# Kernel optimization log

Measured on AMD Instinct MI355X. Metric: run time of the kernel, lower is better.

## Reference

```python
import jax, jax.numpy as jnp
import numpy as np

N_NODES = 20000
N_REL = 16
N_EDGES = 640000
N_HID = 64
N_CLASS = 16
R = 2 * N_REL + 1  # relations after adding inverses + self-loop relation


def setup_inputs() -> dict:
    key = jax.random.key(0)
    k1, k2, k3, k4, k5, k6, k7 = jax.random.split(key, 7)
    src = jax.random.randint(k1, (N_EDGES,), 0, N_NODES)
    rel = jax.random.randint(k2, (N_EDGES,), 0, N_REL)
    dst = jax.random.randint(k3, (N_EDGES,), 0, N_NODES)
    w1 = jax.random.normal(k4, (R, N_NODES, N_HID), dtype=jnp.float32) * 0.02
    b1 = jax.random.normal(k5, (N_HID,), dtype=jnp.float32) * 0.02
    w2 = jax.random.normal(k6, (R, N_HID, N_CLASS), dtype=jnp.float32) * 0.02
    b2 = jax.random.normal(k7, (N_CLASS,), dtype=jnp.float32) * 0.02
    return {"src": src, "rel": rel, "dst": dst, "w1": w1, "b1": b1,
            "w2": w2, "b2": b2, "nnodes": N_NODES, "nrel": N_REL}


def _triples_plus(src, rel, dst, nnodes, nrel):
    # add_inverse_and_self: [original | inverse (r+nrel) | self-loops (r=2*nrel)]
    loop = jnp.arange(nnodes, dtype=src.dtype)
    s = jnp.concatenate([src, dst, loop])
    r = jnp.concatenate([rel, rel + nrel, jnp.full((nnodes,), 2 * nrel, dtype=rel.dtype)])
    o = jnp.concatenate([dst, src, loop])
    return s, r, o


def reference(src, rel, dst, w1, b1, w2, b2, nnodes, nrel):
    E = src.shape[0]
    Rr = 2 * nrel + 1
    RN = Rr * nnodes
    s, r, o = _triples_plus(src, rel, dst, nnodes, nrel)
    ones = jnp.ones(s.shape[0], dtype=jnp.float32)

    # ---- Layer 1: horizontal stacking, featureless ----
    # adj: rows = s, cols = r*N + o; column-wise normalisation with the
    # torch-rgcn sum-swap between original and inverse edge blocks.
    ro = r * nnodes + o
    cnt_ro = jax.ops.segment_sum(ones, ro, num_segments=RN)
    sums = cnt_ro[ro]
    sums = jnp.concatenate([sums[E:2 * E], sums[:E], sums[2 * E:]])
    vals1 = 1.0 / sums
    # output[s] += vals * w1[r, o, :]
    msg1 = vals1[:, None] * w1.reshape(RN, -1)[ro]  # [E_all, nhid]
    h = jax.ops.segment_sum(msg1, s, num_segments=nnodes) + b1
    h = jax.nn.relu(h)

    # ---- Layer 2: vertical stacking ----
    # adj: rows = r*N + s, cols = o; row-wise normalisation.
    rs = r * nnodes + s
    cnt_rs = jax.ops.segment_sum(ones, rs, num_segments=RN)
    vals2 = 1.0 / cnt_rs[rs]
    af = jax.ops.segment_sum(vals2[:, None] * h[o], rs, num_segments=RN)
    af = af.reshape(Rr, nnodes, -1)  # [R, N, nhid]
    out = jnp.einsum('rio,rni->no', w2, af) + b2  # [N, nclass]
    return out
```

## Files before the change

kernel.cpp:

```cpp
#include <hip/hip_runtime.h>

#define NN    20000
#define NRELH 16
#define RTOT  33
#define NHID  64
#define NCLS  16
#define W2PAD 18

typedef unsigned int u32;

__global__ __launch_bounds__(256) void count_kernel(
    const int* __restrict__ src, const int* __restrict__ rel,
    const int* __restrict__ dst, int E,
    int* __restrict__ cntA, int* __restrict__ cntB) {
    int e = blockIdx.x * 256 + threadIdx.x;
    if (e >= E) return;
    int r = rel[e];
    atomicAdd(&cntA[r * NN + dst[e]], 1);
    atomicAdd(&cntB[r * NN + src[e]], 1);
}

__global__ __launch_bounds__(256) void deg_kernel(
    const int* __restrict__ cntA, const int* __restrict__ cntB,
    int* __restrict__ offsets) {
    int n = blockIdx.x * 256 + threadIdx.x;
    if (n >= NN) return;
    int d = 0;
    for (int r = 0; r < NRELH; ++r) d += cntA[r * NN + n] + cntB[r * NN + n];
    offsets[n + 1] = (d + 3) & ~3;
}

__global__ __launch_bounds__(256) void scan_kernel(int* __restrict__ offsets) {
    __shared__ int part[256];
    int t = threadIdx.x;
    const int CH = (NN + 255) / 256;
    int base = t * CH, end = min(base + CH, NN);
    int s = 0;
    for (int n = base; n < end; ++n) s += offsets[n + 1];
    part[t] = s;
    __syncthreads();
    if (t == 0) {
        int run = 0;
        for (int i = 0; i < 256; ++i) { int v = part[i]; part[i] = run; run += v; }
        offsets[0] = 0;
    }
    __syncthreads();
    int run = part[t];
    for (int n = base; n < end; ++n) { run += offsets[n + 1]; offsets[n + 1] = run; }
}

__global__ __launch_bounds__(256) void cursor_pad_kernel(
    const int* __restrict__ cntA, const int* __restrict__ cntB,
    const int* __restrict__ offsets,
    int* __restrict__ curA, int* __restrict__ curB,
    u32* __restrict__ eidx, float* __restrict__ vals) {
    int n = blockIdx.x * 256 + threadIdx.x;
    if (n >= NN) return;
    int p = offsets[n];
    for (int r = 0; r < NRELH; ++r) { curB[r * NN + n] = p; p += cntB[r * NN + n]; }
    for (int r = 0; r < NRELH; ++r) { curA[r * NN + n] = p; p += cntA[r * NN + n]; }
    int pend = offsets[n + 1];
    for (; p < pend; ++p) { eidx[p] = (32u << 15); vals[p] = 0.0f; }
}

__global__ __launch_bounds__(256) void scatter_kernel(
    const int* __restrict__ src, const int* __restrict__ rel,
    const int* __restrict__ dst, int E,
    const int* __restrict__ cntA, const int* __restrict__ cntB,
    int* __restrict__ curA, int* __restrict__ curB,
    u32* __restrict__ eidx, float* __restrict__ vals) {
    int e = blockIdx.x * 256 + threadIdx.x;
    if (e >= E) return;
    int r = rel[e], s0 = src[e], d = dst[e];
    float vb = 1.0f / (float)cntB[r * NN + s0];
    int p1 = atomicAdd(&curB[r * NN + s0], 1);
    eidx[p1] = (u32)d | ((u32)r << 15);
    vals[p1] = vb;
    float va = 1.0f / (float)cntA[r * NN + d];
    int p2 = atomicAdd(&curA[r * NN + d], 1);
    eidx[p2] = (u32)s0 | ((u32)(r + 16) << 15);
    vals[p2] = va;
}

__global__ __launch_bounds__(256) void layer1_gather(
    const u32* __restrict__ eidx, const int* __restrict__ offsets,
    const float* __restrict__ vals,
    const float* __restrict__ w1, const float* __restrict__ b1,
    float* __restrict__ h) {
    int wid  = (blockIdx.x * 256 + threadIdx.x) >> 6;
    int lane = threadIdx.x & 63;
    if (wid >= NN) return;
    int s = wid;
    float acc = w1[(2 * NRELH * NN + s) * NHID + lane];
    int k0 = offsets[s], k1 = offsets[s + 1];
    for (int k = k0; k < k1; k += 4) {
        uint4  e4 = *(const uint4*)&eidx[k];
        float4 v4 = *(const float4*)&vals[k];
        int row0 = (int)(e4.x >> 15) * NN + (int)(e4.x & 0x7FFF);
        int row1 = (int)(e4.y >> 15) * NN + (int)(e4.y & 0x7FFF);
        int row2 = (int)(e4.z >> 15) * NN + (int)(e4.z & 0x7FFF);
        int row3 = (int)(e4.w >> 15) * NN + (int)(e4.w & 0x7FFF);
        float g0 = w1[row0 * NHID + lane];
        float g1 = w1[row1 * NHID + lane];
        float g2 = w1[row2 * NHID + lane];
        float g3 = w1[row3 * NHID + lane];
        acc += v4.x * g0 + v4.y * g1 + v4.z * g2 + v4.w * g3;
    }
    float v = acc + b1[lane];
    h[s * NHID + lane] = v > 0.0f ? v : 0.0f;
}

__global__ __launch_bounds__(1024) void layer2_fold(
    const u32* __restrict__ eidx, const int* __restrict__ offsets,
    const float* __restrict__ vals,
    const float* __restrict__ h, const float* __restrict__ w2,
    const float* __restrict__ b2, float* __restrict__ out) {
    __shared__ float w2L[RTOT * NHID * W2PAD];
    int tid = threadIdx.x;
    for (int idx = tid; idx < RTOT * NHID * NCLS; idx += 1024) {
        int c = idx & 15;
        int ri = idx >> 4;
        w2L[ri * W2PAD + c] = w2[idx];
    }
    __syncthreads();
    int w = tid >> 6, lane = tid & 63;
    for (int s = blockIdx.x * 16 + w; s < NN; s += gridDim.x * 16) {
        float acc16[16];
#pragma unroll
        for (int c = 0; c < 16; ++c) acc16[c] = 0.0f;
        auto FOLD = [&](int r, float a) {
            int b = (r * NHID + lane) * W2PAD;
#pragma unroll
            for (int q = 0; q < 8; ++q) {
                float2 wv = *(const float2*)&w2L[b + 2 * q];
                acc16[2 * q]     += a * wv.x;
                acc16[2 * q + 1] += a * wv.y;
            }
        };
        float hs = h[s * NHID + lane];
        FOLD(32, hs);
        int rcur = 32; float acc = 0.0f;
        int k0 = offsets[s], k1 = offsets[s + 1];
        for (int k = k0; k < k1; k += 4) {
            uint4  e4 = *(const uint4*)&eidx[k];
            float4 v4 = *(const float4*)&vals[k];
            int o0 = e4.x & 0x7FFF, r0 = e4.x >> 15;
            int o1 = e4.y & 0x7FFF, r1 = e4.y >> 15;
            int o2 = e4.z & 0x7FFF, r2 = e4.z >> 15;
            int o3 = e4.w & 0x7FFF, r3 = e4.w >> 15;
            float h0 = h[o0 * NHID + lane];
            float h1 = h[o1 * NHID + lane];
            float h2 = h[o2 * NHID + lane];
            float h3 = h[o3 * NHID + lane];
            if (r0 != rcur) { FOLD(rcur, acc); acc = 0.0f; rcur = r0; } acc += v4.x * h0;
            if (r1 != rcur) { FOLD(rcur, acc); acc = 0.0f; rcur = r1; } acc += v4.y * h1;
            if (r2 != rcur) { FOLD(rcur, acc); acc = 0.0f; rcur = r2; } acc += v4.z * h2;
            if (r3 != rcur) { FOLD(rcur, acc); acc = 0.0f; rcur = r3; } acc += v4.w * h3;
        }
        FOLD(rcur, acc);
        float s8[8];
#pragma unroll
        for (int j = 0; j < 8; ++j) {
            float p0 = __shfl_xor(acc16[2 * j], 1, 64);
            float p1 = __shfl_xor(acc16[2 * j + 1], 1, 64);
            float e0 = acc16[2 * j] + p0, e1 = acc16[2 * j + 1] + p1;
            s8[j] = (lane & 1) ? e1 : e0;
        }
        float s4[4];
#pragma unroll
        for (int j = 0; j < 4; ++j) {
            float p0 = __shfl_xor(s8[2 * j], 2, 64);
            float p1 = __shfl_xor(s8[2 * j + 1], 2, 64);
            float e0 = s8[2 * j] + p0, e1 = s8[2 * j + 1] + p1;
            s4[j] = (lane & 2) ? e1 : e0;
        }
        float s2[2];
#pragma unroll
        for (int j = 0; j < 2; ++j) {
            float p0 = __shfl_xor(s4[2 * j], 4, 64);
            float p1 = __shfl_xor(s4[2 * j + 1], 4, 64);
            float e0 = s4[2 * j] + p0, e1 = s4[2 * j + 1] + p1;
            s2[j] = (lane & 4) ? e1 : e0;
        }
        float p0 = __shfl_xor(s2[0], 8, 64);
        float p1 = __shfl_xor(s2[1], 8, 64);
        float e0 = s2[0] + p0, e1 = s2[1] + p1;
        float t = (lane & 8) ? e1 : e0;
        t += __shfl_xor(t, 16, 64);
        t += __shfl_xor(t, 32, 64);
        if (lane < 16) out[s * NCLS + lane] = t + b2[lane];
    }
}

extern "C" void kernel_launch(void* const* d_in, const int* in_sizes, int n_in,
                              void* d_out, int out_size, void* d_ws, size_t ws_size,
                              hipStream_t stream) {
    const int*   src = (const int*)d_in[0];
    const int*   rel = (const int*)d_in[1];
    const int*   dst = (const int*)d_in[2];
    const float* w1  = (const float*)d_in[3];
    const float* b1  = (const float*)d_in[4];
    const float* w2  = (const float*)d_in[5];
    const float* b2  = (const float*)d_in[6];
    float* out = (float*)d_out;
    const int E = in_sizes[0];
    const int ECAP = 2 * E + 4 * NN;

    int*   cntA    = (int*)d_ws;
    int*   cntB    = cntA + NRELH * NN;
    int*   curA    = cntB + NRELH * NN;
    int*   curB    = curA + NRELH * NN;
    int*   offsets = curB + NRELH * NN;
    u32*   eidx    = (u32*)(offsets + NN + 4);
    float* vals    = (float*)(eidx + ECAP);
    float* h       = vals + ECAP;

    hipMemsetAsync(cntA, 0, (size_t)(2 * NRELH * NN) * 4, stream);

    count_kernel<<<(E + 255) / 256, 256, 0, stream>>>(src, rel, dst, E, cntA, cntB);
    deg_kernel<<<(NN + 255) / 256, 256, 0, stream>>>(cntA, cntB, offsets);
    scan_kernel<<<1, 256, 0, stream>>>(offsets);
    cursor_pad_kernel<<<(NN + 255) / 256, 256, 0, stream>>>(cntA, cntB, offsets,
                                                            curA, curB, eidx, vals);
    scatter_kernel<<<(E + 255) / 256, 256, 0, stream>>>(src, rel, dst, E, cntA, cntB,
                                                        curA, curB, eidx, vals);
    layer1_gather<<<(NN * 64) / 256, 256, 0, stream>>>(eidx, offsets, vals, w1, b1, h);
    layer2_fold<<<256, 1024, 0, stream>>>(eidx, offsets, vals, h, w2, b2, out);
}
```

Measured before the change: 520.9 us.

## Replace CSR scan with atomic bump allocation and interleave edge index/value pairs

The three kernels for degree, single-block scan and cursor setup become one alloc kernel. It reserves each node's padded segment with an atomicAdd on a global counter and stores explicit start and end arrays. This removes the serial one-block scan and two launches. Edge indices and normalisation values are now interleaved as uint2, so the gather kernels fetch both with the same vector loads and the scatter does one 8-byte store per edge. Segment bounds are made wave-uniform with readfirstlane. Node segments are no longer stored in node order, which can reduce locality between neighbouring nodes' edge lists.

Result: faster. 460.5 us (-11.6%).

```diff
diff --git a/kernel.cpp b/kernel.cpp
--- a/kernel.cpp
+++ b/kernel.cpp
@@ -20,47 +20,30 @@
     atomicAdd(&cntB[r * NN + src[e]], 1);
 }
 
-__global__ __launch_bounds__(256) void deg_kernel(
+__global__ __launch_bounds__(256) void alloc_kernel(
     const int* __restrict__ cntA, const int* __restrict__ cntB,
-    int* __restrict__ offsets) {
+    int* __restrict__ gcount,
+    int* __restrict__ curA, int* __restrict__ curB,
+    int* __restrict__ nodeStart, int* __restrict__ nodeEnd,
+    uint2* __restrict__ ent) {
     int n = blockIdx.x * 256 + threadIdx.x;
     if (n >= NN) return;
+    int cb[NRELH], ca[NRELH];
     int d = 0;
-    for (int r = 0; r < NRELH; ++r) d += cntA[r * NN + n] + cntB[r * NN + n];
-    offsets[n + 1] = (d + 3) & ~3;
-}
-
-__global__ __launch_bounds__(256) void scan_kernel(int* __restrict__ offsets) {
-    __shared__ int part[256];
-    int t = threadIdx.x;
-    const int CH = (NN + 255) / 256;
-    int base = t * CH, end = min(base + CH, NN);
-    int s = 0;
-    for (int n = base; n < end; ++n) s += offsets[n + 1];
-    part[t] = s;
-    __syncthreads();
-    if (t == 0) {
-        int run = 0;
-        for (int i = 0; i < 256; ++i) { int v = part[i]; part[i] = run; run += v; }
-        offsets[0] = 0;
-    }
-    __syncthreads();
-    int run = part[t];
-    for (int n = base; n < end; ++n) { run += offsets[n + 1]; offsets[n + 1] = run; }
-}
-
-__global__ __launch_bounds__(256) void cursor_pad_kernel(
-    const int* __restrict__ cntA, const int* __restrict__ cntB,
-    const int* __restrict__ offsets,
-    int* __restrict__ curA, int* __restrict__ curB,
-    u32* __restrict__ eidx, float* __restrict__ vals) {
-    int n = blockIdx.x * 256 + threadIdx.x;
-    if (n >= NN) return;
-    int p = offsets[n];
-    for (int r = 0; r < NRELH; ++r) { curB[r * NN + n] = p; p += cntB[r * NN + n]; }
-    for (int r = 0; r < NRELH; ++r) { curA[r * NN + n] = p; p += cntA[r * NN + n]; }
-    int pend = offsets[n + 1];
-    for (; p < pend; ++p) { eidx[p] = (32u << 15); vals[p] = 0.0f; }
+#pragma unroll
+    for (int r = 0; r < NRELH; ++r) { cb[r] = cntB[r * NN + n]; d += cb[r]; }
+#pragma unroll
+    for (int r = 0; r < NRELH; ++r) { ca[r] = cntA[r * NN + n]; d += ca[r]; }
+    int pdeg = (d + 3) & ~3;
+    int base = atomicAdd(gcount, pdeg);
+    nodeStart[n] = base;
+    nodeEnd[n]   = base + pdeg;
+    int p = base;
+#pragma unroll
+    for (int r = 0; r < NRELH; ++r) { curB[r * NN + n] = p; p += cb[r]; }
+#pragma unroll
+    for (int r = 0; r < NRELH; ++r) { curA[r * NN + n] = p; p += ca[r]; }
+    for (; p < base + pdeg; ++p) ent[p] = make_uint2(32u << 15, 0u);
 }
 
 __global__ __launch_bounds__(256) void scatter_kernel(
@@ -68,51 +51,51 @@
     const int* __restrict__ dst, int E,
     const int* __restrict__ cntA, const int* __restrict__ cntB,
     int* __restrict__ curA, int* __restrict__ curB,
-    u32* __restrict__ eidx, float* __restrict__ vals) {
+    uint2* __restrict__ ent) {
     int e = blockIdx.x * 256 + threadIdx.x;
     if (e >= E) return;
     int r = rel[e], s0 = src[e], d = dst[e];
     float vb = 1.0f / (float)cntB[r * NN + s0];
     int p1 = atomicAdd(&curB[r * NN + s0], 1);
-    eidx[p1] = (u32)d | ((u32)r << 15);
-    vals[p1] = vb;
+    ent[p1] = make_uint2((u32)d | ((u32)r << 15), __float_as_uint(vb));
     float va = 1.0f / (float)cntA[r * NN + d];
     int p2 = atomicAdd(&curA[r * NN + d], 1);
-    eidx[p2] = (u32)s0 | ((u32)(r + 16) << 15);
-    vals[p2] = va;
+    ent[p2] = make_uint2((u32)s0 | ((u32)(r + 16) << 15), __float_as_uint(va));
 }
 
 __global__ __launch_bounds__(256) void layer1_gather(
-    const u32* __restrict__ eidx, const int* __restrict__ offsets,
-    const float* __restrict__ vals,
+    const uint2* __restrict__ ent,
+    const int* __restrict__ nodeStart, const int* __restrict__ nodeEnd,
     const float* __restrict__ w1, const float* __restrict__ b1,
     float* __restrict__ h) {
     int wid  = (blockIdx.x * 256 + threadIdx.x) >> 6;
     int lane = threadIdx.x & 63;
     if (wid >= NN) return;
     int s = wid;
+    int k0 = __builtin_amdgcn_readfirstlane(nodeStart[s]);
+    int k1 = __builtin_amdgcn_readfirstlane(nodeEnd[s]);
     float acc = w1[(2 * NRELH * NN + s) * NHID + lane];
-    int k0 = offsets[s], k1 = offsets[s + 1];
     for (int k = k0; k < k1; k += 4) {
-        uint4  e4 = *(const uint4*)&eidx[k];
-        float4 v4 = *(const float4*)&vals[k];
-        int row0 = (int)(e4.x >> 15) * NN + (int)(e4.x & 0x7FFF);
-        int row1 = (int)(e4.y >> 15) * NN + (int)(e4.y & 0x7FFF);
-        int row2 = (int)(e4.z >> 15) * NN + (int)(e4.z & 0x7FFF);
-        int row3 = (int)(e4.w >> 15) * NN + (int)(e4.w & 0x7FFF);
+        uint4 ea = *(const uint4*)&ent[k];
+        uint4 eb = *(const uint4*)&ent[k + 2];
+        int row0 = (int)(ea.x >> 15) * NN + (int)(ea.x & 0x7FFF);
+        int row1 = (int)(ea.z >> 15) * NN + (int)(ea.z & 0x7FFF);
+        int row2 = (int)(eb.x >> 15) * NN + (int)(eb.x & 0x7FFF);
+        int row3 = (int)(eb.z >> 15) * NN + (int)(eb.z & 0x7FFF);
         float g0 = w1[row0 * NHID + lane];
         float g1 = w1[row1 * NHID + lane];
         float g2 = w1[row2 * NHID + lane];
         float g3 = w1[row3 * NHID + lane];
-        acc += v4.x * g0 + v4.y * g1 + v4.z * g2 + v4.w * g3;
+        acc += __uint_as_float(ea.y) * g0 + __uint_as_float(ea.w) * g1
+             + __uint_as_float(eb.y) * g2 + __uint_as_float(eb.w) * g3;
     }
     float v = acc + b1[lane];
     h[s * NHID + lane] = v > 0.0f ? v : 0.0f;
 }
 
 __global__ __launch_bounds__(1024) void layer2_fold(
-    const u32* __restrict__ eidx, const int* __restrict__ offsets,
-    const float* __restrict__ vals,
+    const uint2* __restrict__ ent,
+    const int* __restrict__ nodeStart, const int* __restrict__ nodeEnd,
     const float* __restrict__ h, const float* __restrict__ w2,
     const float* __restrict__ b2, float* __restrict__ out) {
     __shared__ float w2L[RTOT * NHID * W2PAD];
@@ -140,22 +123,23 @@
         float hs = h[s * NHID + lane];
         FOLD(32, hs);
         int rcur = 32; float acc = 0.0f;
-        int k0 = offsets[s], k1 = offsets[s + 1];
+        int k0 = __builtin_amdgcn_readfirstlane(nodeStart[s]);
+        int k1 = __builtin_amdgcn_readfirstlane(nodeEnd[s]);
         for (int k = k0; k < k1; k += 4) {
-            uint4  e4 = *(const uint4*)&eidx[k];
-            float4 v4 = *(const float4*)&vals[k];
-            int o0 = e4.x & 0x7FFF, r0 = e4.x >> 15;
-            int o1 = e4.y & 0x7FFF, r1 = e4.y >> 15;
-            int o2 = e4.z & 0x7FFF, r2 = e4.z >> 15;
-            int o3 = e4.w & 0x7FFF, r3 = e4.w >> 15;
+            uint4 ea = *(const uint4*)&ent[k];
+            uint4 eb = *(const uint4*)&ent[k + 2];
+            int o0 = ea.x & 0x7FFF, r0 = ea.x >> 15;
+            int o1 = ea.z & 0x7FFF, r1 = ea.z >> 15;
+            int o2 = eb.x & 0x7FFF, r2 = eb.x >> 15;
+            int o3 = eb.z & 0x7FFF, r3 = eb.z >> 15;
             float h0 = h[o0 * NHID + lane];
             float h1 = h[o1 * NHID + lane];
             float h2 = h[o2 * NHID + lane];
             float h3 = h[o3 * NHID + lane];
-            if (r0 != rcur) { FOLD(rcur, acc); acc = 0.0f; rcur = r0; } acc += v4.x * h0;
-            if (r1 != rcur) { FOLD(rcur, acc); acc = 0.0f; rcur = r1; } acc += v4.y * h1;
-            if (r2 != rcur) { FOLD(rcur, acc); acc = 0.0f; rcur = r2; } acc += v4.z * h2;
-            if (r3 != rcur) { FOLD(rcur, acc); acc = 0.0f; rcur = r3; } acc += v4.w * h3;
+            if (r0 != rcur) { FOLD(rcur, acc); acc = 0.0f; rcur = r0; } acc += __uint_as_float(ea.y) * h0;
+            if (r1 != rcur) { FOLD(rcur, acc); acc = 0.0f; rcur = r1; } acc += __uint_as_float(ea.w) * h1;
+            if (r2 != rcur) { FOLD(rcur, acc); acc = 0.0f; rcur = r2; } acc += __uint_as_float(eb.y) * h2;
+            if (r3 != rcur) { FOLD(rcur, acc); acc = 0.0f; rcur = r3; } acc += __uint_as_float(eb.w) * h3;
         }
         FOLD(rcur, acc);
         float s8[8];
@@ -206,24 +190,23 @@
     const int E = in_sizes[0];
     const int ECAP = 2 * E + 4 * NN;
 
-    int*   cntA    = (int*)d_ws;
-    int*   cntB    = cntA + NRELH * NN;
-    int*   curA    = cntB + NRELH * NN;
-    int*   curB    = curA + NRELH * NN;
-    int*   offsets = curB + NRELH * NN;
-    u32*   eidx    = (u32*)(offsets + NN + 4);
-    float* vals    = (float*)(eidx + ECAP);
-    float* h       = vals + ECAP;
-
-    hipMemsetAsync(cntA, 0, (size_t)(2 * NRELH * NN) * 4, stream);
+    int*   cntA      = (int*)d_ws;
+    int*   cntB      = cntA + NRELH * NN;
+    int*   gcount    = cntB + NRELH * NN;
+    int*   curA      = gcount + 4;
+    int*   curB      = curA + NRELH * NN;
+    int*   nodeStart = curB + NRELH * NN;
+    int*   nodeEnd   = nodeStart + NN;
+    uint2* ent       = (uint2*)(nodeEnd + NN);
+    float* h         = (float*)(ent + ECAP);
+
+    hipMemsetAsync(cntA, 0, (size_t)(2 * NRELH * NN + 4) * 4, stream);
 
     count_kernel<<<(E + 255) / 256, 256, 0, stream>>>(src, rel, dst, E, cntA, cntB);
-    deg_kernel<<<(NN + 255) / 256, 256, 0, stream>>>(cntA, cntB, offsets);
-    scan_kernel<<<1, 256, 0, stream>>>(offsets);
-    cursor_pad_kernel<<<(NN + 255) / 256, 256, 0, stream>>>(cntA, cntB, offsets,
-                                                            curA, curB, eidx, vals);
+    alloc_kernel<<<(NN + 255) / 256, 256, 0, stream>>>(cntA, cntB, gcount, curA, curB,
+                                                       nodeStart, nodeEnd, ent);
     scatter_kernel<<<(E + 255) / 256, 256, 0, stream>>>(src, rel, dst, E, cntA, cntB,
-                                                        curA, curB, eidx, vals);
-    layer1_gather<<<(NN * 64) / 256, 256, 0, stream>>>(eidx, offsets, vals, w1, b1, h);
-    layer2_fold<<<256, 1024, 0, stream>>>(eidx, offsets, vals, h, w2, b2, out);
-}
+                                                        curA, curB, ent);
+    layer1_gather<<<(NN * 64) / 256, 256, 0, stream>>>(ent, nodeStart, nodeEnd, w1, b1, h);
+    layer2_fold<<<256, 1024, 0, stream>>>(ent, nodeStart, nodeEnd, h, w2, b2, out);
+}
```
